# Kernel optimization log

Measured on AMD Instinct MI355X. Metric: run time of the kernel, lower is better.

## Reference

```python
import jax, jax.numpy as jnp
import numpy as np

PLP_ORDER = 16
N_CHANNEL = 40
FFT_LENGTH = 512
SAMPLE_RATE = 16000
LIFTER = 22
COMP_FACTOR = 0.33
FLOOR = 1e-5
F_MIN = 0.0
F_MAX = SAMPLE_RATE / 2


def _hz_to_mel(hz):
    return 1127.0 * np.log1p(np.asarray(hz, dtype=np.float64) / 700.0)


def _mel_to_hz(mel):
    return 700.0 * np.expm1(np.asarray(mel, dtype=np.float64) / 1127.0)


def _build_constants():
    # SPTK-style mel filter bank (triangular in mel domain).
    mel_min = _hz_to_mel(F_MIN)
    mel_max = _hz_to_mel(F_MAX)
    lower_bin = max(1, int(F_MIN / SAMPLE_RATE * FFT_LENGTH + 1.5))
    upper_bin = min(FFT_LENGTH // 2, int(F_MAX / SAMPLE_RATE * FFT_LENGTH + 0.5))
    seed = np.arange(1, N_CHANNEL + 2)
    cf_mel = (mel_max - mel_min) / (N_CHANNEL + 1) * seed + mel_min  # (C+1,)
    bins = np.arange(lower_bin, upper_bin)
    mel = _hz_to_mel(SAMPLE_RATE * bins / FFT_LENGTH)
    ch = np.searchsorted(cf_mel, mel, side='left')  # first center freq >= mel
    diff = cf_mel - np.concatenate([[mel_min], cf_mel[:-1]])
    w = (cf_mel[ch] - mel) / diff[ch]
    H = np.zeros((len(bins), N_CHANNEL))
    rows = np.arange(len(bins))
    low = ch - 1
    m_lo = low >= 0
    H[rows[m_lo], low[m_lo]] += w[m_lo]
    m_hi = ch <= N_CHANNEL - 1
    H[rows[m_hi], ch[m_hi]] += 1.0 - w[m_hi]
    # Equal-loudness curve over the first C center frequencies (in Hz).
    cf_hz = _mel_to_hz(cf_mel)
    f2 = cf_hz[:N_CHANNEL] ** 2
    eql = (f2 / (f2 + 160000.0)) ** 2 * (f2 + 1440000.0) / (f2 + 9610000.0)
    # Liftering vector, v[0] = 2.
    m = np.arange(PLP_ORDER + 1)
    lift = 1.0 + LIFTER / 2.0 * np.sin(np.pi / LIFTER * m)
    lift[0] = 2.0
    return lower_bin, upper_bin, H.astype(np.float32), eql.astype(np.float32), lift.astype(np.float32)


LOWER_BIN, UPPER_BIN, H_NP, EQL_NP, LIFT_NP = _build_constants()


def _levinson_durbin(r):
    # r: (..., M+1) autocorrelation -> (gain K, LPC coefficients a_1..a_M)
    M = PLP_ORDER
    E = r[..., 0]
    a = jnp.zeros(r.shape[:-1] + (M,), r.dtype)
    for i in range(1, M + 1):
        acc = r[..., i]
        if i > 1:
            acc = acc + jnp.einsum('...j,...j->...', a[..., : i - 1], r[..., 1:i][..., ::-1])
        k = -acc / E
        if i > 1:
            a = a.at[..., : i - 1].set(a[..., : i - 1] + k[..., None] * a[..., : i - 1][..., ::-1])
        a = a.at[..., i - 1].set(k)
        E = E * (1.0 - k * k)
    return jnp.sqrt(E), a


def _lpc_to_cepstrum(K, a):
    # c0 = log K; c_m = -a_m - sum_{k=1}^{m-1} (k/m) c_k a_{m-k}
    M = PLP_ORDER
    c = [jnp.log(K)]
    for m in range(1, M + 1):
        acc = a[..., m - 1]
        for k in range(1, m):
            acc = acc + (k / m) * c[k] * a[..., m - k - 1]
        c.append(-acc)
    return jnp.stack(c, axis=-1)  # (..., M+1)


def _plp(x):
    H = jnp.asarray(H_NP)
    eql = jnp.asarray(EQL_NP)
    lift = jnp.asarray(LIFT_NP)
    # Mel filter bank on power spectrum (use_power=True)
    fb = jnp.matmul(x[..., LOWER_BIN:UPPER_BIN], H)          # (..., C)
    logfb = jnp.log(jnp.maximum(fb, FLOOR))
    # Equal-loudness scaling + cubic-root amplitude compression
    y = (jnp.exp(logfb) * eql) ** COMP_FACTOR                # (..., C)
    # replicate1: duplicate first and last channels
    y = jnp.concatenate([y[..., :1], y, y[..., -1:]], axis=-1)  # (..., C+2)
    n = y.shape[-1]
    # hfft with norm='forward' -> inverse-FFT-like autocorrelation
    r = jnp.fft.hfft(y) / (2 * (n - 1))
    r = r[..., : PLP_ORDER + 1]
    K, a = _levinson_durbin(r)
    c = _lpc_to_cepstrum(K, a)
    c = c * lift
    return c[..., 1:]  # out_format 'y': PLP without C0, (..., M)


def setup_inputs() -> dict:
    key = jax.random.key(0)
    x = jax.random.uniform(key, (32, 4096, FFT_LENGTH // 2 + 1), dtype=jnp.float32)
    return {"x": x}


def reference(x):
    return _plp(x)
```

## Files before the change

kernel.cpp:

```cpp
#include <hip/hip_runtime.h>

#define NCH    40
#define MORD   16
#define NR     17
#define NBINS  257
#define FPB    128
#define NCHUNK 8
#define PAIRW  65
#define OSTR   21

namespace cfg {

constexpr double PI  = 3.14159265358979323846264338327950288;
constexpr double LN2 = 0.693147180559945309417232121458176568;

constexpr double cexp(double x) {
    double t = 1.0, s = 1.0;
    for (int i = 1; i < 40; ++i) { t *= x / i; s += t; }
    return s;
}

constexpr double clog(double z) {
    double lg = 0.0;
    while (z > 1.4142135623730951) { z *= 0.5; lg += LN2; }
    while (z < 0.7071067811865476) { z *= 2.0; lg -= LN2; }
    double u = (z - 1.0) / (z + 1.0), u2 = u * u, t = u, s = u;
    for (int k = 1; k < 24; ++k) { t *= u2; s += t / (2.0 * k + 1.0); }
    return lg + 2.0 * s;
}

constexpr double ccos(double x) {
    double tp = 2.0 * PI;
    double q = x / tp;
    long long k = (long long)(q + (q >= 0.0 ? 0.5 : -0.5));
    double r = x - (double)k * tp;
    double r2 = r * r, t = 1.0, s = 1.0;
    for (int i = 1; i < 20; ++i) { t *= -r2 / ((2.0 * i - 1.0) * (2.0 * i)); s += t; }
    return s;
}

constexpr double csin(double x) { return ccos(x - PI / 2.0); }

struct Tab {
    int   start[43];
    int   chan[257];
    float w[257];
    float eql[NCH];
    float lift[NR];
    float ctf[NR][21];
    constexpr Tab() : start(), chan(), w(), eql(), lift(), ctf() {
        const double lmax  = clog(87.0 / 7.0);
        const double U1127 = lmax / 41.0;
        for (int c = 0; c <= 41; ++c) {
            double thr = 22.4 * (cexp((double)c * U1127) - 1.0);
            int s = (int)thr + 1;
            if (s < 1) s = 1;
            if (s > 256) s = 256;
            start[c] = s;
        }
        start[42] = start[41];
        for (int c = 0; c <= 40; ++c) {
            for (int b = start[c]; b < start[c + 1]; ++b) {
                double mel = 1127.0 * clog(1.0 + (double)b * 31.25 / 700.0);
                double t   = mel / (1127.0 * U1127);
                w[b] = (float)(t - (double)c);
                chan[b] = c;
            }
        }
        for (int c = 0; c < NCH; ++c) {
            double cf = 700.0 * (cexp((double)(c + 1) * U1127) - 1.0);
            double f2 = cf * cf;
            double e  = f2 / (f2 + 160000.0);
            e = e * e * (f2 + 1440000.0) / (f2 + 9610000.0);
            eql[c] = (float)e;
        }
        for (int m = 0; m < NR; ++m)
            lift[m] = (float)(1.0 + 11.0 * csin(PI * (double)m / 22.0));
        lift[0] = 2.0f;
        for (int l = 0; l < NR; ++l)
            for (int j = 0; j <= 20; ++j) {
                double s = (j == 0) ? 1.0 : 2.0;
                ctf[l][j] = (float)(s * ccos(PI * (double)(j * l) / 41.0) / 82.0);
            }
    }
};

constexpr Tab T{};

}

__device__ __forceinline__ void gload_lds4(const float* g, float* l) {
    __builtin_amdgcn_global_load_lds(
        (const __attribute__((address_space(1))) unsigned int*)g,
        (__attribute__((address_space(3))) unsigned int*)l, 4, 0, 0);
}

__global__ __launch_bounds__(FPB, 2) void plp_kernel(const float* __restrict__ x,
                                                     float* __restrict__ out,
                                                     int nframes)
{
    using cfg::T;
    __shared__ float slab[2][64][PAIRW];

    const int tid = threadIdx.x;
    const long long F0 = (long long)blockIdx.x * FPB;

    const int w = tid >> 6;
    const int l = tid & 63;
    const int s = l >> 5;
    const int j = l & 31;

    auto stage = [&](int c, int b) {
        const float* gp0 = x + (c << 5) + j;
        #pragma unroll
        for (int r = 0; r < 32; ++r) {
            const int g = (w << 5) + r;
            long long fg = F0 + 2 * g + s;
            if (fg > (long long)nframes - 1) fg = (long long)nframes - 1;
            gload_lds4(gp0 + fg * NBINS, &slab[b][g][0]);
        }
    };

    stage(0, 0);

    const int u   = tid >> 1;
    const int v32 = (tid & 1) << 5;

    float fb[NCH];
    #pragma unroll
    for (int c = 0; c < NCH; ++c) fb[c] = 0.f;

    __syncthreads();

    #pragma unroll
    for (int c8 = 0; c8 < NCHUNK; ++c8) {
        if (c8 + 1 < NCHUNK) stage(c8 + 1, (c8 + 1) & 1);
        const float* fr = &slab[c8 & 1][u][v32];
        #pragma unroll
        for (int p = 0; p < 32; ++p) {
            const int bb = (c8 << 5) + p;
            if (bb == 0) continue;
            const float xv = fr[p];
            const int   ch = T.chan[bb];
            const float wa = T.w[bb];
            if (ch < NCH) fb[ch]     = fmaf(wa, xv, fb[ch]);
            if (ch >= 1)  fb[ch - 1] = fmaf(1.0f - wa, xv, fb[ch - 1]);
        }
        if (c8 + 1 < NCHUNK) __syncthreads();
    }

    float yv[NCH];
    #pragma unroll
    for (int c = 0; c < NCH; ++c) {
        float v = fmaxf(fb[c], 1e-5f) * T.eql[c];
        yv[c] = __expf(0.33f * __logf(v));
    }

    float ye[21], yo[21];
    ye[0] = yv[0] + yv[39];  yo[0] = yv[0] - yv[39];
    #pragma unroll
    for (int jj = 1; jj <= 20; ++jj) {
        float aa = yv[jj - 1], bb = yv[40 - jj];
        ye[jj] = aa + bb;  yo[jj] = aa - bb;
    }

    float r[NR];
    #pragma unroll
    for (int lg = 0; lg < NR; ++lg) {
        const float* yy = (lg & 1) ? yo : ye;
        float acc = 0.f;
        #pragma unroll
        for (int jj = 0; jj <= 20; ++jj) acc = fmaf(T.ctf[lg][jj], yy[jj], acc);
        r[lg] = acc;
    }

    float a[MORD];
    #pragma unroll
    for (int i = 0; i < MORD; ++i) a[i] = 0.f;
    float E = r[0];
    #pragma unroll
    for (int i = 1; i <= MORD; ++i) {
        float acc = r[i];
        #pragma unroll
        for (int jj = 0; jj < i - 1; ++jj) acc = fmaf(a[jj], r[i - 1 - jj], acc);
        float k = -acc * __builtin_amdgcn_rcpf(E);
        const int half = (i - 1) / 2;
        #pragma unroll
        for (int jj = 0; jj < half; ++jj) {
            float t1 = a[jj], t2 = a[i - 2 - jj];
            a[jj]         = fmaf(k, t2, t1);
            a[i - 2 - jj] = fmaf(k, t1, t2);
        }
        if ((i - 1) & 1) a[half] = fmaf(k, a[half], a[half]);
        a[i - 1] = k;
        E = E * (1.f - k * k);
    }

    float cc[NR], ccs[NR];
    #pragma unroll
    for (int m = 1; m <= MORD; ++m) {
        float acc = 0.f;
        #pragma unroll
        for (int k2 = 1; k2 < m; ++k2)
            acc = fmaf(ccs[k2], a[m - k2 - 1], acc);
        float cm = -(a[m - 1] + acc * (1.0f / (float)m));
        cc[m]  = cm;
        ccs[m] = (float)m * cm;
    }

    float* ob = &slab[0][0][0];
    #pragma unroll
    for (int m = 1; m <= MORD; ++m)
        ob[tid * OSTR + (m - 1)] = cc[m] * T.lift[m];
    __syncthreads();

    float4* out4 = (float4*)out;
    const long long gbase4 = F0 << 2;
    const long long lim4   = ((long long)nframes) << 2;
    #pragma unroll
    for (int q = 0; q < 4; ++q) {
        const int g4 = (q << 7) + tid;
        const long long gi = gbase4 + g4;
        if (gi < lim4) {
            const int fr2 = g4 >> 2, e = g4 & 3;
            const float* rb = &ob[fr2 * OSTR + (e << 2)];
            out4[gi] = make_float4(rb[0], rb[1], rb[2], rb[3]);
        }
    }
}

extern "C" void kernel_launch(void* const* d_in, const int* in_sizes, int n_in,
                              void* d_out, int out_size, void* d_ws, size_t ws_size,
                              hipStream_t stream) {
    const float* x   = (const float*)d_in[0];
    float*      outp = (float*)d_out;
    int nframes = in_sizes[0] / NBINS;
    int nblocks = (nframes + FPB - 1) / FPB;
    plp_kernel<<<nblocks, FPB, 0, stream>>>(x, outp, nframes);
}
```

Before: 199.7 us.

## Replace LDS-staged loads with per-thread aligned float4 global reads

Removes the shared-memory double-buffered staging of spectrum bins and has each thread load its own frame with float4 reads. Frames are distributed so each wavefront shares one alignment offset (frame mod 4), and a templated path shifts elements to handle the misalignment. Output is stored directly from registers as float4, dropping the LDS transpose and barriers. This relies on cache reuse because adjacent lanes read rows far apart, which may hurt coalescing.

```diff
diff --git a/kernel.cpp b/kernel.cpp
--- a/kernel.cpp
+++ b/kernel.cpp
@@ -4,10 +4,6 @@
 #define MORD   16
 #define NR     17
 #define NBINS  257
-#define FPB    128
-#define NCHUNK 8
-#define PAIRW  65
-#define OSTR   21
 
 namespace cfg {
 
@@ -89,64 +85,58 @@
 
 }
 
-__device__ __forceinline__ void gload_lds4(const float* g, float* l) {
-    __builtin_amdgcn_global_load_lds(
-        (const __attribute__((address_space(1))) unsigned int*)g,
-        (__attribute__((address_space(3))) unsigned int*)l, 4, 0, 0);
-}
-
-__global__ __launch_bounds__(FPB, 2) void plp_kernel(const float* __restrict__ x,
+template<int S>
+__device__ __forceinline__ void fbank_path(const float* __restrict__ x,
+                                           long long fg, float fb[NCH])
+{
+    using cfg::T;
+    const long long B = fg * 257 + 1 - S;
+    const float4* p4 = reinterpret_cast<const float4*>(x + B);
+    float4 a = p4[0];
+    #pragma unroll
+    for (int j = 0; j < 64; ++j) {
+        float4 b;
+        if (S > 0 || j < 63) b = p4[j + 1]; else b = a;
+        float e0, e1, e2, e3;
+        if      (S == 0) { e0 = a.x; e1 = a.y; e2 = a.z; e3 = a.w; }
+        else if (S == 1) { e0 = a.y; e1 = a.z; e2 = a.w; e3 = b.x; }
+        else if (S == 2) { e0 = a.z; e1 = a.w; e2 = b.x; e3 = b.y; }
+        else             { e0 = a.w; e1 = b.x; e2 = b.y; e3 = b.z; }
+        const float ee[4] = { e0, e1, e2, e3 };
+        #pragma unroll
+        for (int q = 0; q < 4; ++q) {
+            const int   bb = 4 * j + 1 + q;
+            const int   ch = T.chan[bb];
+            const float wa = T.w[bb];
+            if (ch < NCH) fb[ch]     = fmaf(wa, ee[q], fb[ch]);
+            if (ch >= 1)  fb[ch - 1] = fmaf(1.0f - wa, ee[q], fb[ch - 1]);
+        }
+        a = b;
+    }
+}
+
+__global__ __launch_bounds__(256, 2) void plp_kernel(const float* __restrict__ x,
                                                      float* __restrict__ out,
                                                      int nframes)
 {
     using cfg::T;
-    __shared__ float slab[2][64][PAIRW];
-
-    const int tid = threadIdx.x;
-    const long long F0 = (long long)blockIdx.x * FPB;
-
-    const int w = tid >> 6;
-    const int l = tid & 63;
-    const int s = l >> 5;
-    const int j = l & 31;
-
-    auto stage = [&](int c, int b) {
-        const float* gp0 = x + (c << 5) + j;
-        #pragma unroll
-        for (int r = 0; r < 32; ++r) {
-            const int g = (w << 5) + r;
-            long long fg = F0 + 2 * g + s;
-            if (fg > (long long)nframes - 1) fg = (long long)nframes - 1;
-            gload_lds4(gp0 + fg * NBINS, &slab[b][g][0]);
-        }
-    };
-
-    stage(0, 0);
-
-    const int u   = tid >> 1;
-    const int v32 = (tid & 1) << 5;
+    const int tid  = threadIdx.x;
+    const int lane = tid & 63;
+    const long long GW = (long long)blockIdx.x * 4 + (tid >> 6);
+    const int       r  = (int)(GW & 3);
+    const long long q  = GW >> 2;
+    const long long fg = (long long)r + 4 * (q * 64 + lane);
+    if (fg >= nframes) return;
 
     float fb[NCH];
     #pragma unroll
     for (int c = 0; c < NCH; ++c) fb[c] = 0.f;
 
-    __syncthreads();
-
-    #pragma unroll
-    for (int c8 = 0; c8 < NCHUNK; ++c8) {
-        if (c8 + 1 < NCHUNK) stage(c8 + 1, (c8 + 1) & 1);
-        const float* fr = &slab[c8 & 1][u][v32];
-        #pragma unroll
-        for (int p = 0; p < 32; ++p) {
-            const int bb = (c8 << 5) + p;
-            if (bb == 0) continue;
-            const float xv = fr[p];
-            const int   ch = T.chan[bb];
-            const float wa = T.w[bb];
-            if (ch < NCH) fb[ch]     = fmaf(wa, xv, fb[ch]);
-            if (ch >= 1)  fb[ch - 1] = fmaf(1.0f - wa, xv, fb[ch - 1]);
-        }
-        if (c8 + 1 < NCHUNK) __syncthreads();
+    switch (r) {
+        case 0:  fbank_path<1>(x, fg, fb); break;
+        case 1:  fbank_path<2>(x, fg, fb); break;
+        case 2:  fbank_path<3>(x, fg, fb); break;
+        default: fbank_path<0>(x, fg, fb); break;
     }
 
     float yv[NCH];
@@ -164,25 +154,25 @@
         ye[jj] = aa + bb;  yo[jj] = aa - bb;
     }
 
-    float r[NR];
+    float rr[NR];
     #pragma unroll
     for (int lg = 0; lg < NR; ++lg) {
         const float* yy = (lg & 1) ? yo : ye;
         float acc = 0.f;
         #pragma unroll
         for (int jj = 0; jj <= 20; ++jj) acc = fmaf(T.ctf[lg][jj], yy[jj], acc);
-        r[lg] = acc;
+        rr[lg] = acc;
     }
 
     float a[MORD];
     #pragma unroll
     for (int i = 0; i < MORD; ++i) a[i] = 0.f;
-    float E = r[0];
+    float E = rr[0];
     #pragma unroll
     for (int i = 1; i <= MORD; ++i) {
-        float acc = r[i];
-        #pragma unroll
-        for (int jj = 0; jj < i - 1; ++jj) acc = fmaf(a[jj], r[i - 1 - jj], acc);
+        float acc = rr[i];
+        #pragma unroll
+        for (int jj = 0; jj < i - 1; ++jj) acc = fmaf(a[jj], rr[i - 1 - jj], acc);
         float k = -acc * __builtin_amdgcn_rcpf(E);
         const int half = (i - 1) / 2;
         #pragma unroll
@@ -208,25 +198,15 @@
         ccs[m] = (float)m * cm;
     }
 
-    float* ob = &slab[0][0][0];
-    #pragma unroll
-    for (int m = 1; m <= MORD; ++m)
-        ob[tid * OSTR + (m - 1)] = cc[m] * T.lift[m];
-    __syncthreads();
-
-    float4* out4 = (float4*)out;
-    const long long gbase4 = F0 << 2;
-    const long long lim4   = ((long long)nframes) << 2;
-    #pragma unroll
-    for (int q = 0; q < 4; ++q) {
-        const int g4 = (q << 7) + tid;
-        const long long gi = gbase4 + g4;
-        if (gi < lim4) {
-            const int fr2 = g4 >> 2, e = g4 & 3;
-            const float* rb = &ob[fr2 * OSTR + (e << 2)];
-            out4[gi] = make_float4(rb[0], rb[1], rb[2], rb[3]);
-        }
-    }
+    float o[16];
+    #pragma unroll
+    for (int m = 1; m <= MORD; ++m) o[m - 1] = cc[m] * T.lift[m];
+
+    float4* op = reinterpret_cast<float4*>(out + (size_t)fg * 16);
+    op[0] = make_float4(o[0],  o[1],  o[2],  o[3]);
+    op[1] = make_float4(o[4],  o[5],  o[6],  o[7]);
+    op[2] = make_float4(o[8],  o[9],  o[10], o[11]);
+    op[3] = make_float4(o[12], o[13], o[14], o[15]);
 }
 
 extern "C" void kernel_launch(void* const* d_in, const int* in_sizes, int n_in,
@@ -235,6 +215,6 @@
     const float* x   = (const float*)d_in[0];
     float*      outp = (float*)d_out;
     int nframes = in_sizes[0] / NBINS;
-    int nblocks = (nframes + FPB - 1) / FPB;
-    plp_kernel<<<nblocks, FPB, 0, stream>>>(x, outp, nframes);
-}
+    int nblocks = (nframes + 255) / 256;
+    plp_kernel<<<nblocks, 256, 0, stream>>>(x, outp, nframes);
+}
```

After: 217.5 us. 1.09x slower.
